# Performance work log

Hardware: AMD Instinct MI355X
Metric: run time of the kernel (lower is better)

The kernel has to match this reference:

```python
import jax, jax.numpy as jnp
import numpy as np

B, S, D, H = 4, 1024, 768, 12
DH = D // H            # 64
MAXPOS = 1024          # config.max_position_embeddings
NTYPES = 8             # flow types (embedding has NTYPES+1 rows, row 0 = padding)


def setup_inputs() -> dict:
    key = jax.random.key(0)
    ks = jax.random.split(key, 12)
    sc = 0.02
    inp = {
        "hidden_states": jax.random.normal(ks[0], (B, S, D), jnp.float32),
        "Wq": jax.random.normal(ks[1], (D, D), jnp.float32) * sc,
        "bq": jnp.zeros((D,), jnp.float32),
        "Wk": jax.random.normal(ks[2], (D, D), jnp.float32) * sc,
        "bk": jnp.zeros((D,), jnp.float32),
        "Wv": jax.random.normal(ks[3], (D, D), jnp.float32) * sc,
        "bv": jnp.zeros((D,), jnp.float32),
        "dist_emb": jax.random.normal(ks[4], (2 * MAXPOS - 1, DH), jnp.float32) * sc,
        "cfg_emb": jax.random.normal(ks[5], (NTYPES + 1, 1), jnp.float32) * sc,
        "dfg_emb": jax.random.normal(ks[6], (NTYPES + 1, 1), jnp.float32) * sc,
        "rfg_emb": jax.random.normal(ks[7], (NTYPES + 1, 1), jnp.float32) * sc,
        "cfg_matrix": jax.random.randint(ks[8], (B, S, S), 0, NTYPES + 1, jnp.int32),
        "dfg_matrix": jax.random.randint(ks[9], (B, S, S), 0, NTYPES + 1, jnp.int32),
        "rdg_matrix": jax.random.randint(ks[10], (B, S, S), 0, NTYPES + 1, jnp.int32),
    }
    return inp


def reference(hidden_states, Wq, bq, Wk, bk, Wv, bv, dist_emb,
              cfg_emb, dfg_emb, rfg_emb, cfg_matrix, dfg_matrix, rdg_matrix):
    b, s, d = hidden_states.shape
    inv_sqrt = 1.0 / float(np.sqrt(DH))

    def heads(x):  # [b,s,d] -> [b,H,s,DH]
        return x.reshape(b, s, H, DH).transpose(0, 2, 1, 3)

    q = heads(hidden_states @ Wq.T + bq)
    k = heads(hidden_states @ Wk.T + bk)
    v = heads(hidden_states @ Wv.T + bv)

    scores = jnp.einsum('bhld,bhrd->bhlr', q, k)

    # relative_key_query positional bias
    dist = jnp.arange(s)[:, None] - jnp.arange(s)[None, :] + (MAXPOS - 1)
    pe = dist_emb[dist]  # [s, s, DH]
    scores = scores + jnp.einsum('bhld,lrd->bhlr', q, pe) \
                    + jnp.einsum('bhrd,lrd->bhlr', k, pe)

    scores = scores * inv_sqrt

    # flow-type bias: scalar embedding per (i,j), padding row 0 forced to zero
    flow = (cfg_emb.at[0].set(0.0)[cfg_matrix][..., 0]
            + dfg_emb.at[0].set(0.0)[dfg_matrix][..., 0]
            + rfg_emb.at[0].set(0.0)[rdg_matrix][..., 0])  # [b,s,s]
    scores = scores + flow[:, None, :, :]

    probs = jax.nn.softmax(scores, axis=-1)
    ctx = jnp.einsum('bhlr,bhrd->bhld', probs, v)
    return ctx.transpose(0, 2, 1, 3).reshape(b, s, d)
```

## Files before the change

kernel.cpp:

```cpp
#include <hip/hip_runtime.h>


typedef __attribute__((ext_vector_type(4))) float f32x4;
typedef __attribute__((ext_vector_type(8))) short s16x8;

#define MFMA_BF16 __builtin_amdgcn_mfma_f32_16x16x32_bf16

__device__ __forceinline__ unsigned short f2bf(float x) {
  unsigned u = __builtin_bit_cast(unsigned, x);
  u += 0x7fffu + ((u >> 16) & 1u);
  return (unsigned short)(u >> 16);
}
__device__ __forceinline__ float bf2f(unsigned short h) {
  unsigned u = ((unsigned)h) << 16;
  return __builtin_bit_cast(float, u);
}
__device__ __forceinline__ float exp2_fast(float x) {
  float r;
  asm("v_exp_f32 %0, %1" : "=v"(r) : "v"(x));
  return r;
}
__device__ __forceinline__ void gl_lds16(const void* g, void* l) {
  __builtin_amdgcn_global_load_lds(
      (const __attribute__((address_space(1))) unsigned int*)g,
      (__attribute__((address_space(3))) unsigned int*)l, 16, 0, 0);
}

__global__ __launch_bounds__(256) void k_prep(
    const float* __restrict__ hs, const float* __restrict__ wq,
    const float* __restrict__ wk, const float* __restrict__ wv,
    const float* __restrict__ de, unsigned short* __restrict__ hsb,
    unsigned short* __restrict__ wb, unsigned short* __restrict__ db) {
  const long HSN = 3145728, WN = 1769472;
  long e = ((long)blockIdx.x * 256 + threadIdx.x) * 4;
  if (e < HSN) {
    float4 v = *(const float4*)(hs + e);
    *(ushort4*)(hsb + e) = make_ushort4(f2bf(v.x), f2bf(v.y), f2bf(v.z), f2bf(v.w));
  } else if (e < HSN + WN) {
    long ew = e - HSN;
    const float* src = (ew >= 1179648) ? wv : ((ew >= 589824) ? wk : wq);
    long off = (ew >= 1179648) ? (ew - 1179648) : ((ew >= 589824) ? (ew - 589824) : ew);
    float4 v = *(const float4*)(src + off);
    *(ushort4*)(wb + ew) = make_ushort4(f2bf(v.x), f2bf(v.y), f2bf(v.z), f2bf(v.w));
  } else {
    long ed = e - HSN - WN;
    ushort4 ov;
    if (ed < 131008) {
      float4 v = *(const float4*)(de + ed);
      ov = make_ushort4(f2bf(v.x), f2bf(v.y), f2bf(v.z), f2bf(v.w));
    } else {
      ov = make_ushort4(0, 0, 0, 0);
    }
    *(ushort4*)(db + ed) = ov;
  }
}

__global__ __launch_bounds__(256) void k_flow(
    const int* __restrict__ cm, const int* __restrict__ dm,
    const int* __restrict__ rm, const float* __restrict__ ce,
    const float* __restrict__ dfe, const float* __restrict__ rfe,
    unsigned short* __restrict__ flT) {
  const int tid = threadIdx.x;
  const int rt = blockIdx.x, lt = blockIdx.y, b = blockIdx.z;
  const int l15 = tid & 15, g = (tid >> 4) & 3, w = tid >> 6;
  const int rowb = lt * 64 + w * 16 + g * 4;
  const int colb = rt * 64 + l15;
  s16x8 o0, o1;
#pragma unroll
  for (int n = 0; n < 4; ++n) {
#pragma unroll
    for (int r = 0; r < 4; ++r) {
      const long idx = ((long)b << 20) + ((long)(rowb + r) << 10) + colb + (n << 4);
      const int c = cm[idx], d = dm[idx], rr = rm[idx];
      const float v = (c ? ce[c] : 0.f) + (d ? dfe[d] : 0.f) + (rr ? rfe[rr] : 0.f);
      const short hv = (short)f2bf(1.4426950408889634f * v);
      if (n < 2) o0[n * 4 + r] = hv; else o1[(n - 2) * 4 + r] = hv;
    }
  }
  unsigned short* dst =
      flT + ((long)((((b << 4) + lt) << 4) | rt) << 12) + (tid << 4);
  *(s16x8*)(dst) = o0;
  *(s16x8*)(dst + 8) = o1;
}

__global__ __launch_bounds__(256) void k_qkv(
    const unsigned short* __restrict__ A, const unsigned short* __restrict__ W,
    const float* __restrict__ bq, const float* __restrict__ bk,
    const float* __restrict__ bv, unsigned short* __restrict__ Qp,
    unsigned short* __restrict__ Kp, unsigned short* __restrict__ Vp) {
  __shared__ __align__(16) char smq[16384];
  char* sa = smq;
  char* sb = smq + 8192;
  const int tid = threadIdx.x, w = tid >> 6, lane = tid & 63;
  const int g = lane >> 4, l15 = lane & 15;
  const int n0 = blockIdx.x * 128, m0 = blockIdx.y * 128;
  const int wm = w >> 1, wn = w & 1;
  f32x4 acc[4][4] = {};
  for (int k0 = 0; k0 < 768; k0 += 32) {
#pragma unroll
    for (int it = 0; it < 2; ++it) {
      const int c = (w << 7) + (it << 6) + lane;
      const int row = c >> 2, sl = c & 3;
      const int so = ((sl ^ ((row >> 1) & 3)) << 3);
      char* dst = smq + ((w << 7) + (it << 6)) * 16;
      gl_lds16(A + (long)(m0 + row) * 768 + k0 + so, dst);
      gl_lds16(W + (long)(n0 + row) * 768 + k0 + so, dst + 8192);
    }
    __syncthreads();
    s16x8 af[4], bf[4];
#pragma unroll
    for (int mi = 0; mi < 4; ++mi) {
      const int row = wm * 64 + mi * 16 + l15;
      af[mi] = *(const s16x8*)(sa + row * 64 + ((g ^ ((row >> 1) & 3)) << 4));
    }
#pragma unroll
    for (int ni = 0; ni < 4; ++ni) {
      const int row = wn * 64 + ni * 16 + l15;
      bf[ni] = *(const s16x8*)(sb + row * 64 + ((g ^ ((row >> 1) & 3)) << 4));
    }
#pragma unroll
    for (int mi = 0; mi < 4; ++mi)
#pragma unroll
      for (int ni = 0; ni < 4; ++ni)
        acc[mi][ni] = MFMA_BF16(af[mi], bf[ni], acc[mi][ni], 0, 0, 0);
    __syncthreads();
  }
  const int t_sel = n0 / 768;
  const float* bias = (t_sel == 0) ? bq : (t_sel == 1) ? bk : bv;
  unsigned short* dst = (t_sel == 0) ? Qp : (t_sel == 1) ? Kp : Vp;
#pragma unroll
  for (int ni = 0; ni < 4; ++ni) {
    const int mcol = n0 + wn * 64 + ni * 16 + l15;
    const int nw2 = mcol - t_sel * 768;
    const float bvv = bias[nw2];
    const int h = nw2 >> 6, dh = nw2 & 63;
#pragma unroll
    for (int mi = 0; mi < 4; ++mi) {
#pragma unroll
      for (int r = 0; r < 4; ++r) {
        const int token = m0 + wm * 64 + mi * 16 + (g << 2) + r;
        const int b = token >> 10, s = token & 1023;
        const long idx = ((((long)(b * 12 + h)) << 10) + s) * 64 + dh;
        dst[idx] = f2bf(acc[mi][ni][r] + bvv);
      }
    }
  }
}

__global__ __launch_bounds__(256) void k_vt(const unsigned short* __restrict__ Vp,
                                            unsigned short* __restrict__ Vt) {
  __shared__ __align__(16) unsigned short t[64][64];
  const int bh = blockIdx.y, s0 = blockIdx.x * 64;
  const int tid = threadIdx.x;
#pragma unroll
  for (int it = 0; it < 2; ++it) {
    const int c = it * 256 + tid;
    const int row = c >> 3, sl = c & 7;
    const int slot = sl ^ ((row >> 3) & 7);
    s16x8 v = *(const s16x8*)(Vp + (((long)bh << 10) + s0 + row) * 64 + sl * 8);
    *(s16x8*)&t[row][slot * 8] = v;
  }
  __syncthreads();
#pragma unroll
  for (int it = 0; it < 2; ++it) {
    const int c = it * 256 + tid;
    const int d = c >> 3, ss = c & 7;
    const int cg = d >> 3;
    s16x8 vv;
#pragma unroll
    for (int i = 0; i < 8; ++i) {
      const int rr = ss * 8 + i;
      vv[i] = (short)t[rr][((cg ^ ((rr >> 3) & 7)) << 3) + (d & 7)];
    }
    *(s16x8*)(Vt + (((long)bh * 64 + d) << 10) + s0 + ss * 8) = vv;
  }
}

__global__ __launch_bounds__(256, 3) void k_attn(
    const unsigned short* __restrict__ Qp, const unsigned short* __restrict__ Kp,
    const unsigned short* __restrict__ Vtp, const unsigned short* __restrict__ Db,
    const unsigned short* __restrict__ FlT, float* __restrict__ Out) {
  __shared__ __align__(16) char sm[50688];
  char* Kl = sm;
  char* Vl = sm + 8192;
  char* Dl = sm + 16384;
  unsigned short* KDs = (unsigned short*)(sm + 32768);
  char* Pl = sm + 41472;

  const int tid = threadIdx.x, w = tid >> 6, lane = tid & 63;
  const int g = lane >> 4, l15 = lane & 15;
  const int l0 = blockIdx.x << 6, h = blockIdx.y, b = blockIdx.z;
  const int bh = b * 12 + h;
  const unsigned short* Qb = Qp + ((long)bh << 16);
  const unsigned short* Kb = Kp + ((long)bh << 16);
  const unsigned short* Vb = Vtp + ((long)bh << 16);
  const unsigned short* fTb =
      FlT + ((long)(((b << 4) + blockIdx.x) << 4) << 12) + (tid << 4);

  const int qrow = l0 + (w << 4) + l15;
  const s16x8 qf0 = *(const s16x8*)(Qb + (long)qrow * 64 + g * 8);
  const s16x8 qf1 = *(const s16x8*)(Qb + (long)qrow * 64 + 32 + g * 8);

  int srcad[4];
  bool msk[4];
#pragma unroll
  for (int r = 0; r < 4; ++r) {
    const int bl = ((g << 2) + r - 1) & 15;
    srcad[r] = (((lane & 48) + ((bl - l15) & 15)) << 2);
    msk[r] = (l15 <= bl);
  }
  const bool g0 = (g == 0);

  f32x4 oacc[4] = {};
  float lpart[4] = {0.f, 0.f, 0.f, 0.f};

  for (int rt = 0; rt < 16; ++rt) {
    const int r0 = rt << 6;
    const int t0 = l0 - r0 + 960;

    const s16x8 fv0 = *(const s16x8*)(fTb + ((long)rt << 12));
    const s16x8 fv1 = *(const s16x8*)(fTb + ((long)rt << 12) + 8);

#pragma unroll
    for (int it = 0; it < 2; ++it) {
      const int c = (w << 7) + (it << 6) + lane;
      const int row = c >> 3, sl = c & 7;
      const int so = ((sl ^ (row & 7)) << 3);
      char* dst = sm + ((w << 7) + (it << 6)) * 16;
      gl_lds16(Kb + (long)(r0 + row) * 64 + so, dst);
      gl_lds16(Vb + (long)row * 1024 + r0 + so, dst + 8192);
    }
    {
      const int nh = (rt == 0) ? 2 : 1;
      for (int hh = 0; hh < nh; ++hh) {
        const int ts = t0 + (hh << 6);
        char* dhalf = Dl + (((ts >> 6) & 1) << 13);
#pragma unroll
        for (int it = 0; it < 2; ++it) {
          const int c = (w << 7) + (it << 6) + lane;
          const int row = c >> 3, sl = c & 7;
          gl_lds16(Db + (long)(ts + row) * 64 + ((sl ^ (row & 7)) << 3),
                   dhalf + ((w << 7) + (it << 6)) * 16);
        }
      }
    }
    __syncthreads();

    f32x4 qa[5];
#pragma unroll
    for (int lt = 0; lt < 5; ++lt) {
      const int nq = w + lt;
      const int pb = ((((t0 >> 6) + (nq >> 2)) & 1) << 6) + ((nq & 3) << 4);
      const int trow = pb + l15;
      const s16x8 d0 = *(const s16x8*)(Dl + trow * 128 + ((g ^ (trow & 7)) << 4));
      const s16x8 d1 = *(const s16x8*)(Dl + trow * 128 + (((4 + g) ^ (trow & 7)) << 4));
      f32x4 a = {};
      a = MFMA_BF16(qf0, d0, a, 0, 0, 0);
      a = MFMA_BF16(qf1, d1, a, 0, 0, 0);
      qa[lt] = a;
    }

    {
      const int krow = (w << 4) + l15;
      const s16x8 kf0 = *(const s16x8*)(Kl + krow * 128 + ((g ^ (krow & 7)) << 4));
      const s16x8 kf1 = *(const s16x8*)(Kl + krow * 128 + (((4 + g) ^ (krow & 7)) << 4));
#pragma unroll
      for (int kt = 0; kt < 5; ++kt) {
        const int nk = 3 - w + kt;
        const int pb = ((((t0 >> 6) + (nk >> 2)) & 1) << 6) + ((nk & 3) << 4);
        const int trow = pb + l15;
        const s16x8 d0 = *(const s16x8*)(Dl + trow * 128 + ((g ^ (trow & 7)) << 4));
        const s16x8 d1 = *(const s16x8*)(Dl + trow * 128 + (((4 + g) ^ (trow & 7)) << 4));
        f32x4 ka = {};
        ka = MFMA_BF16(kf0, d0, ka, 0, 0, 0);
        ka = MFMA_BF16(kf1, d1, ka, 0, 0, 0);
#pragma unroll
        for (int r = 0; r < 4; ++r) {
          const int prow = (w << 4) + (g << 2) + r;
          const int ck = (kt << 4) + l15 + (g << 2) + r - 15;
          if (kt == 0 || kt == 4) {
            if ((unsigned)ck < 64u) KDs[prow * 68 + ck] = f2bf(ka[r]);
          } else {
            KDs[prow * 68 + ck] = f2bf(ka[r]);
          }
        }
      }
    }
    __syncthreads();

    f32x4 sacc[4] = {};
#pragma unroll
    for (int n = 0; n < 4; ++n) {
      const int kr = (n << 4) + l15;
      const s16x8 b0 = *(const s16x8*)(Kl + kr * 128 + ((g ^ (kr & 7)) << 4));
      const s16x8 b1 = *(const s16x8*)(Kl + kr * 128 + (((4 + g) ^ (kr & 7)) << 4));
      sacc[n] = MFMA_BF16(qf0, b0, sacc[n], 0, 0, 0);
      sacc[n] = MFMA_BF16(qf1, b1, sacc[n], 0, 0, 0);
    }
#pragma unroll
    for (int n = 0; n < 4; ++n) {
#pragma unroll
      for (int r = 0; r < 4; ++r) {
        const int ib = (w << 4) + (g << 2) + r;
        const int j = (n << 4) + l15;
        float hi, lo;
        if (r == 0) {
          hi = g0 ? qa[3 - n][0] : qa[4 - n][0];
          lo = qa[3 - n][0];
        } else {
          hi = qa[4 - n][r];
          lo = qa[3 - n][r];
        }
        const float vsrc = msk[r] ? hi : lo;
        const float qd = __builtin_bit_cast(
            float, __builtin_amdgcn_ds_bpermute(
                       srcad[r], __builtin_bit_cast(int, vsrc)));
        const float kd = bf2f(KDs[j * 68 + ib]);
        const float fv = bf2f((unsigned short)(
            n < 2 ? fv0[(n << 2) + r] : fv1[((n - 2) << 2) + r]));
        sacc[n][r] = (sacc[n][r] + qd + kd) * 0.18033688f + fv;
      }
    }

#pragma unroll
    for (int r = 0; r < 4; ++r) {
      const float p0 = exp2_fast(sacc[0][r]);
      const float p1 = exp2_fast(sacc[1][r]);
      const float p2 = exp2_fast(sacc[2][r]);
      const float p3 = exp2_fast(sacc[3][r]);
      sacc[0][r] = p0; sacc[1][r] = p1; sacc[2][r] = p2; sacc[3][r] = p3;
      lpart[r] += (p0 + p1) + (p2 + p3);
    }

#pragma unroll
    for (int n = 0; n < 4; ++n) {
#pragma unroll
      for (int r = 0; r < 4; ++r) {
        const int ib = (w << 4) + (g << 2) + r;
        const int j = (n << 4) + l15;
        *(unsigned short*)(Pl + ib * 144 + (((j >> 3) ^ (ib & 7)) << 4) +
                           ((j & 7) << 1)) = f2bf(sacc[n][r]);
      }
    }

#pragma unroll
    for (int k0 = 0; k0 < 2; ++k0) {
      const int prow = (w << 4) + l15;
      const s16x8 pf = *(const s16x8*)(
          Pl + prow * 144 + ((((k0 << 2) + g) ^ (prow & 7)) << 4));
#pragma unroll
      for (int n = 0; n < 4; ++n) {
        const int vrow = (n << 4) + l15;
        const s16x8 vf = *(const s16x8*)(
            Vl + vrow * 128 + ((((k0 << 2) + g) ^ (vrow & 7)) << 4));
        oacc[n] = MFMA_BF16(pf, vf, oacc[n], 0, 0, 0);
      }
    }
    __syncthreads();
  }

  float lsum[4];
#pragma unroll
  for (int r = 0; r < 4; ++r) {
    float s = lpart[r];
#pragma unroll
    for (int dd = 1; dd < 16; dd <<= 1) s += __shfl_xor(s, dd, 64);
    lsum[r] = s;
  }
#pragma unroll
  for (int n = 0; n < 4; ++n) {
#pragma unroll
    for (int r = 0; r < 4; ++r) {
      const int l = l0 + (w << 4) + (g << 2) + r;
      const int d = (n << 4) + l15;
      Out[((long)(b * 1024 + l)) * 768 + h * 64 + d] = oacc[n][r] / lsum[r];
    }
  }
}

extern "C" void kernel_launch(void* const* d_in, const int* in_sizes, int n_in,
                              void* d_out, int out_size, void* d_ws, size_t ws_size,
                              hipStream_t stream) {
  const float* hs = (const float*)d_in[0];
  const float* Wq = (const float*)d_in[1];
  const float* bq = (const float*)d_in[2];
  const float* Wk = (const float*)d_in[3];
  const float* bk = (const float*)d_in[4];
  const float* Wv = (const float*)d_in[5];
  const float* bv = (const float*)d_in[6];
  const float* de = (const float*)d_in[7];
  const float* ce = (const float*)d_in[8];
  const float* dfe = (const float*)d_in[9];
  const float* rfe = (const float*)d_in[10];
  const int* cm = (const int*)d_in[11];
  const int* dm = (const int*)d_in[12];
  const int* rm = (const int*)d_in[13];
  float* out = (float*)d_out;
  char* ws = (char*)d_ws;

  unsigned short* hsb = (unsigned short*)(ws + 0);
  unsigned short* wb  = (unsigned short*)(ws + 6291456);
  unsigned short* db  = (unsigned short*)(ws + 9830400);
  unsigned short* flT = (unsigned short*)(ws + 10092544);
  unsigned short* qp  = (unsigned short*)(ws + 18481152);
  unsigned short* kp  = (unsigned short*)(ws + 24772608);
  unsigned short* vp  = (unsigned short*)(ws + 31064064);
  unsigned short* vt  = (unsigned short*)(ws + 37355520);

  k_prep<<<4928, 256, 0, stream>>>(hs, Wq, Wk, Wv, de, hsb, wb, db);
  k_flow<<<dim3(16, 16, 4), 256, 0, stream>>>(cm, dm, rm, ce, dfe, rfe, flT);
  k_qkv<<<dim3(18, 32), 256, 0, stream>>>(hsb, wb, bq, bk, bv, qp, kp, vp);
  k_vt<<<dim3(16, 48), 256, 0, stream>>>(vp, vt);
  k_attn<<<dim3(16, 12, 4), 256, 0, stream>>>(qp, kp, vt, db, flT, out);
}
```

Before: 114.6 us.

## Prefetch next K/V tile into registers and overlap distance-embedding loads

The first K, V and distance-embedding tiles are loaded before the loop. Each iteration then prefetches the next K/V tile into registers and writes it to LDS at the end of the iteration. The next distance-embedding half is issued with async global-to-LDS loads after the second barrier, so global latency overlaps with compute. This adds a barrier per iteration and extra register pressure, and the rt+1 wraparound causes one redundant fetch.

```diff
diff --git a/kernel.cpp b/kernel.cpp
--- a/kernel.cpp
+++ b/kernel.cpp
@@ -197,6 +197,25 @@
   const unsigned short* fTb =
       FlT + ((long)(((b << 4) + blockIdx.x) << 4) << 12) + (tid << 4);
 
+  const int c0 = (w << 7) + lane, c1 = c0 + 64;
+  const int row0 = c0 >> 3, sl0 = c0 & 7, so0 = ((sl0 ^ (row0 & 7)) << 3);
+  const int row1 = c1 >> 3, sl1 = c1 & 7, so1 = ((sl1 ^ (row1 & 7)) << 3);
+
+  gl_lds16(Kb + (long)row0 * 64 + so0, sm + c0 * 16);
+  gl_lds16(Kb + (long)row1 * 64 + so1, sm + c1 * 16);
+  gl_lds16(Vb + (long)row0 * 1024 + so0, sm + 8192 + c0 * 16);
+  gl_lds16(Vb + (long)row1 * 1024 + so1, sm + 8192 + c1 * 16);
+  {
+    const int t00 = l0 + 960;
+#pragma unroll
+    for (int hh = 0; hh < 2; ++hh) {
+      const int ts = t00 + (hh << 6);
+      char* dhalf = Dl + (((ts >> 6) & 1) << 13);
+      gl_lds16(Db + (long)(ts + row0) * 64 + so0, dhalf + c0 * 16);
+      gl_lds16(Db + (long)(ts + row1) * 64 + so1, dhalf + c1 * 16);
+    }
+  }
+
   const int qrow = l0 + (w << 4) + l15;
   const s16x8 qf0 = *(const s16x8*)(Qb + (long)qrow * 64 + g * 8);
   const s16x8 qf1 = *(const s16x8*)(Qb + (long)qrow * 64 + 32 + g * 8);
@@ -214,37 +233,20 @@
   f32x4 oacc[4] = {};
   float lpart[4] = {0.f, 0.f, 0.f, 0.f};
 
+  __syncthreads();
+
   for (int rt = 0; rt < 16; ++rt) {
     const int r0 = rt << 6;
     const int t0 = l0 - r0 + 960;
 
+    const int rp0 = ((rt + 1) & 15) << 6;
+    const s16x8 kpr0 = *(const s16x8*)(Kb + (long)(rp0 + row0) * 64 + so0);
+    const s16x8 kpr1 = *(const s16x8*)(Kb + (long)(rp0 + row1) * 64 + so1);
+    const s16x8 vpr0 = *(const s16x8*)(Vb + (long)row0 * 1024 + rp0 + so0);
+    const s16x8 vpr1 = *(const s16x8*)(Vb + (long)row1 * 1024 + rp0 + so1);
+
     const s16x8 fv0 = *(const s16x8*)(fTb + ((long)rt << 12));
     const s16x8 fv1 = *(const s16x8*)(fTb + ((long)rt << 12) + 8);
-
-#pragma unroll
-    for (int it = 0; it < 2; ++it) {
-      const int c = (w << 7) + (it << 6) + lane;
-      const int row = c >> 3, sl = c & 7;
-      const int so = ((sl ^ (row & 7)) << 3);
-      char* dst = sm + ((w << 7) + (it << 6)) * 16;
-      gl_lds16(Kb + (long)(r0 + row) * 64 + so, dst);
-      gl_lds16(Vb + (long)row * 1024 + r0 + so, dst + 8192);
-    }
-    {
-      const int nh = (rt == 0) ? 2 : 1;
-      for (int hh = 0; hh < nh; ++hh) {
-        const int ts = t0 + (hh << 6);
-        char* dhalf = Dl + (((ts >> 6) & 1) << 13);
-#pragma unroll
-        for (int it = 0; it < 2; ++it) {
-          const int c = (w << 7) + (it << 6) + lane;
-          const int row = c >> 3, sl = c & 7;
-          gl_lds16(Db + (long)(ts + row) * 64 + ((sl ^ (row & 7)) << 3),
-                   dhalf + ((w << 7) + (it << 6)) * 16);
-        }
-      }
-    }
-    __syncthreads();
 
     f32x4 qa[5];
 #pragma unroll
@@ -288,6 +290,13 @@
     }
     __syncthreads();
 
+    if (rt < 15) {
+      const int ts = t0 - 64;
+      char* dhalf = Dl + (((ts >> 6) & 1) << 13);
+      gl_lds16(Db + (long)(ts + row0) * 64 + so0, dhalf + c0 * 16);
+      gl_lds16(Db + (long)(ts + row1) * 64 + so1, dhalf + c1 * 16);
+    }
+
     f32x4 sacc[4] = {};
 #pragma unroll
     for (int n = 0; n < 4; ++n) {
@@ -301,8 +310,6 @@
     for (int n = 0; n < 4; ++n) {
 #pragma unroll
       for (int r = 0; r < 4; ++r) {
-        const int ib = (w << 4) + (g << 2) + r;
-        const int j = (n << 4) + l15;
         float hi, lo;
         if (r == 0) {
           hi = g0 ? qa[3 - n][0] : qa[4 - n][0];
@@ -315,6 +322,8 @@
         const float qd = __builtin_bit_cast(
             float, __builtin_amdgcn_ds_bpermute(
                        srcad[r], __builtin_bit_cast(int, vsrc)));
+        const int ib = (w << 4) + (g << 2) + r;
+        const int j = (n << 4) + l15;
         const float kd = bf2f(KDs[j * 68 + ib]);
         const float fv = bf2f((unsigned short)(
             n < 2 ? fv0[(n << 2) + r] : fv1[((n - 2) << 2) + r]));
@@ -356,6 +365,12 @@
         oacc[n] = MFMA_BF16(pf, vf, oacc[n], 0, 0, 0);
       }
     }
+    __syncthreads();
+
+    *(s16x8*)(sm + c0 * 16) = kpr0;
+    *(s16x8*)(sm + c1 * 16) = kpr1;
+    *(s16x8*)(sm + 8192 + c0 * 16) = vpr0;
+    *(s16x8*)(sm + 8192 + c1 * 16) = vpr1;
     __syncthreads();
   }
 
```

Measured after the change: 115.6 us. Within noise of the previous version (+0.8%).
